# Optimization experiments

Hardware: AMD Instinct MI355X
Metric: run time of the kernel (lower is better)

The kernel has to match this reference:

```python
import jax, jax.numpy as jnp
import numpy as np

HIDDEN = 10
ACTIONS = 6
NUM_LAYERS = 19
IN_CH = 64
LSTM_IN = HIDDEN + 2
EPS = 1e-5
DN = ('NCHW', 'OIHW', 'NCHW')


def _bn(x, g, b):
    # BatchNorm2d in training mode: per-batch stats over (N,H,W), biased variance
    m = x.mean((0, 2, 3), keepdims=True)
    v = x.var((0, 2, 3), keepdims=True)
    return (x - m) * jax.lax.rsqrt(v + EPS) * g[None, :, None, None] + b[None, :, None, None]


def _conv_dw(x, dw_w, ga, ba, pw_w, gb, bb):
    c = x.shape[1]
    x = jax.lax.conv_general_dilated(x, dw_w, (2, 2), [(1, 1), (1, 1)],
                                     feature_group_count=c, dimension_numbers=DN)
    x = jax.nn.relu(_bn(x, ga, ba))
    x = jax.lax.conv_general_dilated(x, pw_w, (1, 1), 'VALID', dimension_numbers=DN)
    return jax.nn.relu(_bn(x, gb, bb))


def _lstm_cell(xt, h, c, wih, whh, bih, bhh):
    # torch gate order: i, f, g, o
    gates = xt @ wih.T + bih + h @ whh.T + bhh
    i, f, g, o = jnp.split(gates, 4, axis=1)
    c = jax.nn.sigmoid(f) * c + jax.nn.sigmoid(i) * jnp.tanh(g)
    h = jax.nn.sigmoid(o) * jnp.tanh(c)
    return h, c


def setup_inputs() -> dict:
    key = jax.random.key(0)
    ks = iter(jax.random.split(key, 32))
    n = lambda shape, s=0.1: jax.random.normal(next(ks), shape, dtype=jnp.float32) * s
    d = {
        'x': jax.random.normal(next(ks), (256, IN_CH, 56, 56), dtype=jnp.float32),
        # block 0: 64 -> 10
        'dw0_w': n((IN_CH, 1, 3, 3)), 'bn0a_g': jnp.ones((IN_CH,)), 'bn0a_b': jnp.zeros((IN_CH,)),
        'pw0_w': n((HIDDEN, IN_CH, 1, 1)), 'bn0b_g': jnp.ones((HIDDEN,)), 'bn0b_b': jnp.zeros((HIDDEN,)),
        # blocks 1..3: 10 -> 10 (stacked)
        'dwr_w': n((3, HIDDEN, 1, 3, 3)), 'bnra_g': jnp.ones((3, HIDDEN)), 'bnra_b': jnp.zeros((3, HIDDEN)),
        'pwr_w': n((3, HIDDEN, HIDDEN, 1, 1)), 'bnrb_g': jnp.ones((3, HIDDEN)), 'bnrb_b': jnp.zeros((3, HIDDEN)),
        # 2-layer LSTM
        'wih0': n((4 * HIDDEN, LSTM_IN)), 'whh0': n((4 * HIDDEN, HIDDEN)),
        'bih0': n((4 * HIDDEN,)), 'bhh0': n((4 * HIDDEN,)),
        'wih1': n((4 * HIDDEN, HIDDEN)), 'whh1': n((4 * HIDDEN, HIDDEN)),
        'bih1': n((4 * HIDDEN,)), 'bhh1': n((4 * HIDDEN,)),
        # hidden2logits
        'head_w': n((2 * ACTIONS, HIDDEN)), 'head_b': n((2 * ACTIONS,)),
    }
    return d


def reference(x, dw0_w, bn0a_g, bn0a_b, pw0_w, bn0b_g, bn0b_b,
              dwr_w, bnra_g, bnra_b, pwr_w, bnrb_g, bnrb_b,
              wih0, whh0, bih0, bhh0, wih1, whh1, bih1, bhh1,
              head_w, head_b):
    # reduce: 4 conv_dw blocks + global avg pool -> [B, HIDDEN]
    f = _conv_dw(x, dw0_w, bn0a_g, bn0a_b, pw0_w, bn0b_g, bn0b_b)
    for i in range(3):
        f = _conv_dw(f, dwr_w[i], bnra_g[i], bnra_b[i], pwr_w[i], bnrb_g[i], bnrb_b[i])
    feat = f.mean((2, 3))  # [B, HIDDEN]
    B = feat.shape[0]
    z = jnp.zeros((B, HIDDEN), feat.dtype)
    key0 = jax.random.key(1)

    def step(carry, _):
        h0, c0, h1, c1, subseq, key = carry
        inp = jnp.concatenate([feat, subseq], axis=1)  # [B, 12]
        h0, c0 = _lstm_cell(inp, h0, c0, wih0, whh0, bih0, bhh0)
        h1, c1 = _lstm_cell(h0, h1, c1, wih1, whh1, bih1, bhh1)
        logits = h1 @ head_w.T + head_b  # [B, 2*ACTIONS]
        logits_a, logits_w = logits[:, :ACTIONS], logits[:, ACTIONS:]
        key, ka, kw = jax.random.split(key, 3)
        bit_a = jax.random.categorical(ka, logits_a, axis=1)
        bit_w = jax.random.categorical(kw, logits_w, axis=1)
        lpa = jnp.take_along_axis(jax.nn.log_softmax(logits_a, axis=1), bit_a[:, None], axis=1)[:, 0]
        lpw = jnp.take_along_axis(jax.nn.log_softmax(logits_w, axis=1), bit_w[:, None], axis=1)[:, 0]
        subseq = jnp.stack([bit_a, bit_w], axis=1).astype(feat.dtype)  # [B, 2]
        return (h0, c0, h1, c1, subseq, key), (bit_a, bit_w, lpa, lpw)

    carry0 = (z, z, z, z, jnp.zeros((B, 2), feat.dtype), key0)
    _, (bit_a, bit_w, lpa, lpw) = jax.lax.scan(step, carry0, None, length=NUM_LAYERS)
    # [T, B] -> [B, T]
    return ((bit_a.T + 2, bit_w.T + 2), (lpa.T, lpw.T))
```

## Files before the change

### kernel.cpp

```cpp
#include <hip/hip_runtime.h>
#include <stdint.h>
#include <math.h>

#define TF_ROUND(r) do { x0 += x1; x1 = (x1 << (r)) | (x1 >> (32 - (r))); x1 ^= x0; } while (0)

__device__ __forceinline__ void threefry2x32(uint32_t k0, uint32_t k1,
                                             uint32_t x0, uint32_t x1,
                                             uint32_t& y0, uint32_t& y1)
{
    uint32_t k2 = k0 ^ k1 ^ 0x1BD11BDAu;
    x0 += k0; x1 += k1;
    TF_ROUND(13); TF_ROUND(15); TF_ROUND(26); TF_ROUND(6);
    x0 += k1; x1 += k2 + 1u;
    TF_ROUND(17); TF_ROUND(29); TF_ROUND(16); TF_ROUND(24);
    x0 += k2; x1 += k0 + 2u;
    TF_ROUND(13); TF_ROUND(15); TF_ROUND(26); TF_ROUND(6);
    x0 += k0; x1 += k1 + 3u;
    TF_ROUND(17); TF_ROUND(29); TF_ROUND(16); TF_ROUND(24);
    x0 += k1; x1 += k2 + 4u;
    TF_ROUND(13); TF_ROUND(15); TF_ROUND(26); TF_ROUND(6);
    y0 = x0 + k2; y1 = x1 + k0 + 5u;
}

__device__ __forceinline__ void wave_red2(double& s, double& q) {
    for (int off = 32; off > 0; off >>= 1) {
        s += __shfl_down(s, off);
        q += __shfl_down(q, off);
    }
}

__device__ __forceinline__ float sigf(float x) { return 0.5f + 0.5f * tanhf(0.5f * x); }

__global__ __launch_bounds__(256) void dw0_kernel(
    const float* __restrict__ in, const float* __restrict__ wts,
    float* __restrict__ out, double* __restrict__ psum)
{
    __shared__ float tile[3136];
    __shared__ double sred[8];
    const int tid = threadIdx.x, lane = tid & 63, wid = tid >> 6;
    const int blk = blockIdx.x;
    const int n = blk >> 6, c = blk & 63;

    const float4* ip4 = (const float4*)(in + (size_t)blk * 3136);
    float4* tp4 = (float4*)tile;
#pragma unroll
    for (int r = 0; r < 3; ++r) tp4[tid + r * 256] = ip4[tid + r * 256];
    if (tid < 16) tp4[768 + tid] = ip4[768 + tid];
    float w9[9];
#pragma unroll
    for (int k = 0; k < 9; ++k) w9[k] = wts[c * 9 + k];
    __syncthreads();

    double ls = 0.0, lq = 0.0;
    if (tid < 196) {
        const int oh = tid / 7, ow0 = (tid - oh * 7) * 4;
        const int col0 = 2 * ow0 - 1;
        float rv[3][9];
#pragma unroll
        for (int kh = 0; kh < 3; ++kh) {
            const int ih = 2 * oh - 1 + kh;
            if (ih >= 0) {
                const float* rp = tile + ih * 56 + col0;
                rv[kh][0] = (col0 >= 0) ? rp[0] : 0.f;
#pragma unroll
                for (int j = 1; j < 9; ++j) rv[kh][j] = rp[j];
            } else {
#pragma unroll
                for (int j = 0; j < 9; ++j) rv[kh][j] = 0.f;
            }
        }
        float a0 = 0.f, a1 = 0.f, a2 = 0.f, a3 = 0.f;
#pragma unroll
        for (int kh = 0; kh < 3; ++kh)
#pragma unroll
            for (int kw = 0; kw < 3; ++kw) {
                const float w = w9[kh * 3 + kw];
                a0 = fmaf(rv[kh][0 + kw], w, a0);
                a1 = fmaf(rv[kh][2 + kw], w, a1);
                a2 = fmaf(rv[kh][4 + kw], w, a2);
                a3 = fmaf(rv[kh][6 + kw], w, a3);
            }
        *(float4*)(out + (size_t)blk * 784 + oh * 28 + ow0) = make_float4(a0, a1, a2, a3);
        ls = (double)a0 + (double)a1 + (double)a2 + (double)a3;
        lq = (double)a0 * a0 + (double)a1 * a1 + (double)a2 * a2 + (double)a3 * a3;
    }
    wave_red2(ls, lq);
    if (lane == 0) { sred[wid] = ls; sred[4 + wid] = lq; }
    __syncthreads();
    if (tid == 0) {
        psum[c * 256 + n] = sred[0] + sred[1] + sred[2] + sred[3];
        psum[16384 + c * 256 + n] = sred[4] + sred[5] + sred[6] + sred[7];
    }
}

__global__ __launch_bounds__(256) void red_chan(
    const double* __restrict__ psum, int NB, double count,
    const float* __restrict__ g, const float* __restrict__ b,
    float2* __restrict__ stats, int C)
{
    __shared__ double sred[8];
    const int c = blockIdx.x, tid = threadIdx.x, lane = tid & 63, wid = tid >> 6;
    double s = 0.0, q = 0.0;
    for (int i = tid; i < NB; i += 256) {
        s += psum[(size_t)c * NB + i];
        q += psum[(size_t)C * NB + (size_t)c * NB + i];
    }
    wave_red2(s, q);
    if (lane == 0) { sred[wid] = s; sred[4 + wid] = q; }
    __syncthreads();
    if (tid == 0) {
        double ss = sred[0] + sred[1] + sred[2] + sred[3];
        double qq = sred[4] + sred[5] + sred[6] + sred[7];
        double mean = ss / count;
        double var = qq / count - mean * mean;
        double A = (1.0 / sqrt(var + 1e-5)) * (double)g[c];
        stats[c] = make_float2((float)A, (float)((double)b[c] - mean * A));
    }
}

__global__ __launch_bounds__(256) void pw0_kernel(
    const float* __restrict__ in, const float* __restrict__ wts,
    const float2* __restrict__ st0, float* __restrict__ out,
    double* __restrict__ psum)
{
    __shared__ float sw[640];
    __shared__ float2 sst[64];
    __shared__ double srs[10][4], srq[10][4];
    const int tid = threadIdx.x, lane = tid & 63, wid = tid >> 6;
    for (int i = tid; i < 640; i += 256) sw[i] = wts[i];
    if (tid < 64) sst[tid] = st0[tid];
    __syncthreads();

    const int p = blockIdx.x * 256 + tid;
    const int n = p / 196, sp4 = p - n * 196;
    const float4* ip4 = (const float4*)in + (size_t)n * 12544 + sp4;
    float4 acc[10];
#pragma unroll
    for (int oc = 0; oc < 10; ++oc) acc[oc] = make_float4(0.f, 0.f, 0.f, 0.f);
#pragma unroll 8
    for (int c = 0; c < 64; ++c) {
        float4 v = ip4[c * 196];
        const float2 stc = sst[c];
        v.x = fmaxf(fmaf(v.x, stc.x, stc.y), 0.f);
        v.y = fmaxf(fmaf(v.y, stc.x, stc.y), 0.f);
        v.z = fmaxf(fmaf(v.z, stc.x, stc.y), 0.f);
        v.w = fmaxf(fmaf(v.w, stc.x, stc.y), 0.f);
#pragma unroll
        for (int oc = 0; oc < 10; ++oc) {
            const float wv = sw[oc * 64 + c];
            acc[oc].x = fmaf(v.x, wv, acc[oc].x);
            acc[oc].y = fmaf(v.y, wv, acc[oc].y);
            acc[oc].z = fmaf(v.z, wv, acc[oc].z);
            acc[oc].w = fmaf(v.w, wv, acc[oc].w);
        }
    }
#pragma unroll
    for (int oc = 0; oc < 10; ++oc)
        ((float4*)out)[(size_t)(n * 10 + oc) * 196 + sp4] = acc[oc];

#pragma unroll
    for (int oc = 0; oc < 10; ++oc) {
        double s = (double)acc[oc].x + (double)acc[oc].y + (double)acc[oc].z + (double)acc[oc].w;
        double q = (double)acc[oc].x * acc[oc].x + (double)acc[oc].y * acc[oc].y
                 + (double)acc[oc].z * acc[oc].z + (double)acc[oc].w * acc[oc].w;
        wave_red2(s, q);
        if (lane == 0) { srs[oc][wid] = s; srq[oc][wid] = q; }
    }
    __syncthreads();
    if (tid < 10) {
        psum[tid * 196 + blockIdx.x] = srs[tid][0] + srs[tid][1] + srs[tid][2] + srs[tid][3];
        psum[1960 + tid * 196 + blockIdx.x] = srq[tid][0] + srq[tid][1] + srq[tid][2] + srq[tid][3];
    }
}

__global__ __launch_bounds__(256) void dw_mid(
    const float* __restrict__ in, const float* __restrict__ wts,
    const float2* __restrict__ stIn, float* __restrict__ out,
    double* __restrict__ psum)
{
    __shared__ float tile[784];
    __shared__ double sred[8];
    const int tid = threadIdx.x, lane = tid & 63, wid = tid >> 6;
    const int blk = blockIdx.x;
    const int n = blk / 10, c = blk - n * 10;
    const float2 stc = stIn[c];
    float w9[9];
#pragma unroll
    for (int k = 0; k < 9; ++k) w9[k] = wts[c * 9 + k];

    const float4* ip4 = (const float4*)(in + (size_t)blk * 784);
    if (tid < 196) {
        float4 v = ip4[tid];
        v.x = fmaxf(fmaf(v.x, stc.x, stc.y), 0.f);
        v.y = fmaxf(fmaf(v.y, stc.x, stc.y), 0.f);
        v.z = fmaxf(fmaf(v.z, stc.x, stc.y), 0.f);
        v.w = fmaxf(fmaf(v.w, stc.x, stc.y), 0.f);
        ((float4*)tile)[tid] = v;
    }
    __syncthreads();

    double ls = 0.0, lq = 0.0;
    if (tid < 196) {
        const int oh = tid / 14, ow = tid - oh * 14;
        float acc = 0.f;
#pragma unroll
        for (int kh = 0; kh < 3; ++kh) {
            const int ih = 2 * oh - 1 + kh;
            if (ih < 0) continue;
#pragma unroll
            for (int kw = 0; kw < 3; ++kw) {
                const int iw = 2 * ow - 1 + kw;
                if (iw < 0) continue;
                acc = fmaf(tile[ih * 28 + iw], w9[kh * 3 + kw], acc);
            }
        }
        out[(size_t)blk * 196 + tid] = acc;
        ls = (double)acc; lq = (double)acc * (double)acc;
    }
    wave_red2(ls, lq);
    if (lane == 0) { sred[wid] = ls; sred[4 + wid] = lq; }
    __syncthreads();
    if (tid == 0) {
        psum[c * 256 + n] = sred[0] + sred[1] + sred[2] + sred[3];
        psum[2560 + c * 256 + n] = sred[4] + sred[5] + sred[6] + sred[7];
    }
}

__global__ __launch_bounds__(256) void pw_mid4(
    const float* __restrict__ in, const float* __restrict__ wts,
    const float2* __restrict__ stIn, float* __restrict__ out,
    double* __restrict__ psum)
{
    __shared__ float sw[100];
    __shared__ float2 sst[10];
    __shared__ double srs[10][4], srq[10][4];
    const int tid = threadIdx.x, lane = tid & 63, wid = tid >> 6;
    if (tid < 100) sw[tid] = wts[tid];
    if (tid < 10) sst[tid] = stIn[tid];
    __syncthreads();

    const int p = blockIdx.x * 256 + tid;
    const int n = p / 49, q = p - n * 49;
    const float4* ip4 = (const float4*)in + (size_t)n * 490 + q;
    float4 acc[10];
#pragma unroll
    for (int oc = 0; oc < 10; ++oc) acc[oc] = make_float4(0.f, 0.f, 0.f, 0.f);
#pragma unroll
    for (int c = 0; c < 10; ++c) {
        float4 v = ip4[c * 49];
        const float2 stc = sst[c];
        v.x = fmaxf(fmaf(v.x, stc.x, stc.y), 0.f);
        v.y = fmaxf(fmaf(v.y, stc.x, stc.y), 0.f);
        v.z = fmaxf(fmaf(v.z, stc.x, stc.y), 0.f);
        v.w = fmaxf(fmaf(v.w, stc.x, stc.y), 0.f);
#pragma unroll
        for (int oc = 0; oc < 10; ++oc) {
            const float wv = sw[oc * 10 + c];
            acc[oc].x = fmaf(v.x, wv, acc[oc].x);
            acc[oc].y = fmaf(v.y, wv, acc[oc].y);
            acc[oc].z = fmaf(v.z, wv, acc[oc].z);
            acc[oc].w = fmaf(v.w, wv, acc[oc].w);
        }
    }
#pragma unroll
    for (int oc = 0; oc < 10; ++oc)
        ((float4*)out)[(size_t)n * 490 + oc * 49 + q] = acc[oc];

#pragma unroll
    for (int oc = 0; oc < 10; ++oc) {
        double s = (double)acc[oc].x + (double)acc[oc].y + (double)acc[oc].z + (double)acc[oc].w;
        double qq = (double)acc[oc].x * acc[oc].x + (double)acc[oc].y * acc[oc].y
                  + (double)acc[oc].z * acc[oc].z + (double)acc[oc].w * acc[oc].w;
        wave_red2(s, qq);
        if (lane == 0) { srs[oc][wid] = s; srq[oc][wid] = qq; }
    }
    __syncthreads();
    if (tid < 10) {
        psum[tid * 49 + blockIdx.x] = srs[tid][0] + srs[tid][1] + srs[tid][2] + srs[tid][3];
        psum[490 + tid * 49 + blockIdx.x] = srq[tid][0] + srq[tid][1] + srq[tid][2] + srq[tid][3];
    }
}

template<int HIN, int HOUT>
__global__ __launch_bounds__(64) void dw_small(
    const float* __restrict__ in, const float* __restrict__ wts,
    const float2* __restrict__ stIn, float* __restrict__ out,
    double* __restrict__ psum)
{
    constexpr int ISZ = HIN * HIN, OSZ = HOUT * HOUT;
    constexpr bool UP = (2 * (HOUT - 1) + 1) >= HIN;
    const int lane = threadIdx.x;
    const int blk = blockIdx.x;
    const int n = blk / 10, c = blk - n * 10;
    const float2 stc = stIn[c];
    float w9[9];
#pragma unroll
    for (int k = 0; k < 9; ++k) w9[k] = wts[c * 9 + k];
    const float* ip = in + (size_t)blk * ISZ;

    double s = 0.0, q = 0.0;
    if (lane < OSZ) {
        const int oh = lane / HOUT, ow = lane - oh * HOUT;
        float acc = 0.f;
#pragma unroll
        for (int kh = 0; kh < 3; ++kh) {
            const int ih = 2 * oh - 1 + kh;
            if (ih < 0) continue;
            if (UP && ih >= HIN) continue;
#pragma unroll
            for (int kw = 0; kw < 3; ++kw) {
                const int iw = 2 * ow - 1 + kw;
                if (iw < 0) continue;
                if (UP && iw >= HIN) continue;
                const float v = fmaxf(fmaf(ip[ih * HIN + iw], stc.x, stc.y), 0.f);
                acc = fmaf(v, w9[kh * 3 + kw], acc);
            }
        }
        out[(size_t)blk * OSZ + lane] = acc;
        s = (double)acc; q = (double)acc * (double)acc;
    }
    wave_red2(s, q);
    if (lane == 0) { psum[c * 256 + n] = s; psum[2560 + c * 256 + n] = q; }
}

template<int S>
__global__ __launch_bounds__(256) void pw_sc(
    const float* __restrict__ in, const float* __restrict__ wts,
    const float2* __restrict__ stIn, float* __restrict__ out,
    double* __restrict__ psum)
{
    __shared__ float sw[100];
    __shared__ float2 sst[10];
    __shared__ double srs[10][4], srq[10][4];
    const int tid = threadIdx.x, lane = tid & 63, wid = tid >> 6;
    if (tid < 100) sw[tid] = wts[tid];
    if (tid < 10) sst[tid] = stIn[tid];
    __syncthreads();

    const int p = blockIdx.x * 256 + tid;
    const int n = p / S, px = p - n * S;
    const float* ip = in + (size_t)n * 10 * S + px;
    float v[10];
#pragma unroll
    for (int c = 0; c < 10; ++c)
        v[c] = fmaxf(fmaf(ip[c * S], sst[c].x, sst[c].y), 0.f);
    float* op = out + (size_t)n * 10 * S + px;
    double ds[10], dq[10];
#pragma unroll
    for (int oc = 0; oc < 10; ++oc) {
        float a = 0.f;
#pragma unroll
        for (int c = 0; c < 10; ++c) a = fmaf(v[c], sw[oc * 10 + c], a);
        op[oc * S] = a;
        ds[oc] = (double)a; dq[oc] = (double)a * (double)a;
    }
#pragma unroll
    for (int oc = 0; oc < 10; ++oc) {
        double s = ds[oc], q = dq[oc];
        wave_red2(s, q);
        if (lane == 0) { srs[oc][wid] = s; srq[oc][wid] = q; }
    }
    __syncthreads();
    if (tid < 10) {
        const int G = gridDim.x;
        psum[tid * G + blockIdx.x] = srs[tid][0] + srs[tid][1] + srs[tid][2] + srs[tid][3];
        psum[10 * G + tid * G + blockIdx.x] = srq[tid][0] + srq[tid][1] + srq[tid][2] + srq[tid][3];
    }
}

__global__ __launch_bounds__(64) void rollout_kernel(
    const float* __restrict__ t7, const float2* __restrict__ st7,
    const float* __restrict__ wih0, const float* __restrict__ whh0,
    const float* __restrict__ bih0, const float* __restrict__ bhh0,
    const float* __restrict__ wih1, const float* __restrict__ whh1,
    const float* __restrict__ bih1, const float* __restrict__ bhh1,
    const float* __restrict__ head_w, const float* __restrict__ head_b,
    float* __restrict__ out)
{
    const int bb = blockIdx.x;
    const int l = threadIdx.x;
    __shared__ float gum[2][19][6];
    __shared__ float s_inp[12], s_h0[10], s_h1[10], s_gates[40], s_logits[12];

    {
        uint32_t k0 = 0u, k1 = 1u;
        const uint32_t m = (uint32_t)(l < 3 ? l : 0);
        for (int t = 0; t < 19; ++t) {
            uint32_t y0, y1;
            threefry2x32(k0, k1, 0u, m, y0, y1);
            const uint32_t nk0 = (uint32_t)__shfl((int)y0, 0);
            const uint32_t nk1 = (uint32_t)__shfl((int)y1, 0);
            const uint32_t ka0 = (uint32_t)__shfl((int)y0, 1);
            const uint32_t ka1 = (uint32_t)__shfl((int)y1, 1);
            const uint32_t kw0 = (uint32_t)__shfl((int)y0, 2);
            const uint32_t kw1 = (uint32_t)__shfl((int)y1, 2);
            if (l < 12) {
                const int path = l / 6;
                const int j = l - path * 6;
                const uint32_t kk0 = path ? kw0 : ka0;
                const uint32_t kk1 = path ? kw1 : ka1;
                const uint32_t flat = (uint32_t)(bb * 6 + j);
                uint32_t z0, z1;
                threefry2x32(kk0, kk1, 0u, flat, z0, z1);
                const uint32_t bits = z0 ^ z1;
                float u = __uint_as_float((bits >> 9) | 0x3f800000u) - 1.0f;
                if (u == 0.0f) u = 1.17549435e-38f;
                const double l1 = log((double)u);
                gum[path][t][j] = (float)(-log(-l1));
            }
            k0 = nk0; k1 = nk1;
        }
    }

    if (l < 10) {
        const float2 stc = st7[l];
        const float* tp = t7 + (size_t)(bb * 10 + l) * 16;
        float f = 0.f;
#pragma unroll
        for (int i = 0; i < 16; ++i) f += fmaxf(fmaf(tp[i], stc.x, stc.y), 0.f);
        s_inp[l] = f * 0.0625f;
        s_h0[l] = 0.f; s_h1[l] = 0.f;
    }
    if (l >= 10 && l < 12) s_inp[l] = 0.f;

    float wi0[12], wh0[10], bs0 = 0.f;
    float wi1[10], wh1[10], bs1 = 0.f;
    float hwr[10], hbr = 0.f;
    if (l < 40) {
#pragma unroll
        for (int k = 0; k < 12; ++k) wi0[k] = wih0[l * 12 + k];
#pragma unroll
        for (int k = 0; k < 10; ++k) wh0[k] = whh0[l * 10 + k];
        bs0 = bih0[l] + bhh0[l];
#pragma unroll
        for (int k = 0; k < 10; ++k) wi1[k] = wih1[l * 10 + k];
#pragma unroll
        for (int k = 0; k < 10; ++k) wh1[k] = whh1[l * 10 + k];
        bs1 = bih1[l] + bhh1[l];
    }
    if (l < 12) {
#pragma unroll
        for (int k = 0; k < 10; ++k) hwr[k] = head_w[l * 10 + k];
        hbr = head_b[l];
    }

    float c0 = 0.f, c1v = 0.f;
    __syncthreads();

    for (int t = 0; t < 19; ++t) {
        if (l < 40) {
            float gacc = bs0;
#pragma unroll
            for (int k = 0; k < 12; ++k) gacc = fmaf(s_inp[k], wi0[k], gacc);
#pragma unroll
            for (int k = 0; k < 10; ++k) gacc = fmaf(s_h0[k], wh0[k], gacc);
            s_gates[l] = gacc;
        }
        __syncthreads();
        if (l < 10) {
            const float gi = s_gates[l], gf = s_gates[10 + l], gg = s_gates[20 + l], go = s_gates[30 + l];
            c0 = sigf(gf) * c0 + sigf(gi) * tanhf(gg);
            s_h0[l] = sigf(go) * tanhf(c0);
        }
        __syncthreads();
        if (l < 40) {
            float gacc = bs1;
#pragma unroll
            for (int k = 0; k < 10; ++k) gacc = fmaf(s_h0[k], wi1[k], gacc);
#pragma unroll
            for (int k = 0; k < 10; ++k) gacc = fmaf(s_h1[k], wh1[k], gacc);
            s_gates[l] = gacc;
        }
        __syncthreads();
        if (l < 10) {
            const float gi = s_gates[l], gf = s_gates[10 + l], gg = s_gates[20 + l], go = s_gates[30 + l];
            c1v = sigf(gf) * c1v + sigf(gi) * tanhf(gg);
            s_h1[l] = sigf(go) * tanhf(c1v);
        }
        __syncthreads();
        if (l < 12) {
            float v = hbr;
#pragma unroll
            for (int k = 0; k < 10; ++k) v = fmaf(s_h1[k], hwr[k], v);
            s_logits[l] = v;
        }
        __syncthreads();
        if (l < 2) {
            const float* lg = &s_logits[l * 6];
            const float* gm = &gum[l][t][0];
            int best = 0; float bv = lg[0] + gm[0];
#pragma unroll
            for (int j = 1; j < 6; ++j) { const float v = lg[j] + gm[j]; if (v > bv) { bv = v; best = j; } }
            float mx = lg[0];
#pragma unroll
            for (int j = 1; j < 6; ++j) mx = fmaxf(mx, lg[j]);
            float se = 0.f;
#pragma unroll
            for (int j = 0; j < 6; ++j) se += expf(lg[j] - mx);
            const float lp = (lg[best] - mx) - logf(se);
            out[l * 4864 + bb * 19 + t] = (float)(best + 2);
            out[9728 + l * 4864 + bb * 19 + t] = lp;
            s_inp[10 + l] = (float)best;
        }
        __syncthreads();
    }
}

extern "C" void kernel_launch(void* const* d_in, const int* in_sizes, int n_in,
                              void* d_out, int out_size, void* d_ws, size_t ws_size,
                              hipStream_t stream)
{
    const float* x      = (const float*)d_in[0];
    const float* dw0_w  = (const float*)d_in[1];
    const float* bn0a_g = (const float*)d_in[2];
    const float* bn0a_b = (const float*)d_in[3];
    const float* pw0_w  = (const float*)d_in[4];
    const float* bn0b_g = (const float*)d_in[5];
    const float* bn0b_b = (const float*)d_in[6];
    const float* dwr_w  = (const float*)d_in[7];
    const float* bnra_g = (const float*)d_in[8];
    const float* bnra_b = (const float*)d_in[9];
    const float* pwr_w  = (const float*)d_in[10];
    const float* bnrb_g = (const float*)d_in[11];
    const float* bnrb_b = (const float*)d_in[12];
    const float* wih0   = (const float*)d_in[13];
    const float* whh0   = (const float*)d_in[14];
    const float* bih0   = (const float*)d_in[15];
    const float* bhh0   = (const float*)d_in[16];
    const float* wih1   = (const float*)d_in[17];
    const float* whh1   = (const float*)d_in[18];
    const float* bih1   = (const float*)d_in[19];
    const float* bhh1   = (const float*)d_in[20];
    const float* head_w = (const float*)d_in[21];
    const float* head_b = (const float*)d_in[22];
    float* out = (float*)d_out;

    char* ws = (char*)d_ws;
    size_t off = 0;
    auto take = [&](size_t bytes) -> char* {
        char* p = ws + off;
        off += (bytes + 255) & ~(size_t)255;
        return p;
    };
    float* y0     = (float*)take(12845056ull * 4);
    float* t1     = (float*)take(2007040ull * 4);
    float* t2     = (float*)take(501760ull * 4);
    float* t3     = (float*)take(501760ull * 4);
    float* t4     = (float*)take(125440ull * 4);
    float* t5     = (float*)take(125440ull * 4);
    float* t6     = (float*)take(40960ull * 4);
    float* t7     = (float*)take(40960ull * 4);
    double* psumA = (double*)take(32768ull * 8);
    double* psumB = (double*)take(3920ull * 8);
    double* psumC = (double*)take(5120ull * 8);
    double* psumD = (double*)take(980ull * 8);
    double* psumE = (double*)take(5120ull * 8);
    double* psumF = (double*)take(980ull * 8);
    double* psumG = (double*)take(5120ull * 8);
    double* psumH = (double*)take(320ull * 8);
    float2* st0   = (float2*)take(64 * sizeof(float2));
    float2* st1   = (float2*)take(16 * sizeof(float2));
    float2* st2   = (float2*)take(16 * sizeof(float2));
    float2* st3   = (float2*)take(16 * sizeof(float2));
    float2* st4   = (float2*)take(16 * sizeof(float2));
    float2* st5   = (float2*)take(16 * sizeof(float2));
    float2* st6   = (float2*)take(16 * sizeof(float2));
    float2* st7   = (float2*)take(16 * sizeof(float2));

    dw0_kernel<<<16384, 256, 0, stream>>>(x, dw0_w, y0, psumA);
    red_chan<<<64, 256, 0, stream>>>(psumA, 256, 200704.0, bn0a_g, bn0a_b, st0, 64);
    pw0_kernel<<<196, 256, 0, stream>>>(y0, pw0_w, st0, t1, psumB);
    red_chan<<<10, 256, 0, stream>>>(psumB, 196, 200704.0, bn0b_g, bn0b_b, st1, 10);
    dw_mid<<<2560, 256, 0, stream>>>(t1, dwr_w, st1, t2, psumC);
    red_chan<<<10, 256, 0, stream>>>(psumC, 256, 50176.0, bnra_g, bnra_b, st2, 10);
    pw_mid4<<<49, 256, 0, stream>>>(t2, pwr_w, st2, t3, psumD);
    red_chan<<<10, 256, 0, stream>>>(psumD, 49, 50176.0, bnrb_g, bnrb_b, st3, 10);
    dw_small<14, 7><<<2560, 64, 0, stream>>>(t3, dwr_w + 90, st3, t4, psumE);
    red_chan<<<10, 256, 0, stream>>>(psumE, 256, 12544.0, bnra_g + 10, bnra_b + 10, st4, 10);
    pw_sc<49><<<49, 256, 0, stream>>>(t4, pwr_w + 100, st4, t5, psumF);
    red_chan<<<10, 256, 0, stream>>>(psumF, 49, 12544.0, bnrb_g + 10, bnrb_b + 10, st5, 10);
    dw_small<7, 4><<<2560, 64, 0, stream>>>(t5, dwr_w + 180, st5, t6, psumG);
    red_chan<<<10, 256, 0, stream>>>(psumG, 256, 4096.0, bnra_g + 20, bnra_b + 20, st6, 10);
    pw_sc<16><<<16, 256, 0, stream>>>(t6, pwr_w + 200, st6, t7, psumH);
    red_chan<<<10, 256, 0, stream>>>(psumH, 16, 4096.0, bnrb_g + 20, bnrb_b + 20, st7, 10);
    rollout_kernel<<<256, 64, 0, stream>>>(t7, st7, wih0, whh0, bih0, bhh0,
                                           wih1, whh1, bih1, bhh1, head_w, head_b, out);
}
```

Baseline: 161.4 us.

## Fold BN statistic reductions into consumer kernels, dropping seven red_chan launches

Each downstream kernel now reduces the producer's per-block partial sums itself and computes the BN scale and shift locally, so the separate red_chan launches between stages go away. This removes seven small kernel launches and their serialization gaps on the stream. In exchange, every block (up to 2560 per stage) redundantly re-reads and reduces up to a few hundred doubles of partial sums, which adds latency at the start of each block.

Measured after the change: 164.6 us. No clear change (+2.0%).

```diff
diff --git a/kernel.cpp b/kernel.cpp
--- a/kernel.cpp
+++ b/kernel.cpp
@@ -173,28 +173,47 @@
     }
 }
 
-__global__ __launch_bounds__(256) void dw_mid(
+__global__ __launch_bounds__(256) void dw_mid_f(
     const float* __restrict__ in, const float* __restrict__ wts,
-    const float2* __restrict__ stIn, float* __restrict__ out,
-    double* __restrict__ psum)
+    const double* __restrict__ psumIn,
+    const float* __restrict__ g, const float* __restrict__ b,
+    float* __restrict__ out, double* __restrict__ psum)
 {
     __shared__ float tile[784];
     __shared__ double sred[8];
+    __shared__ float sAB[2];
     const int tid = threadIdx.x, lane = tid & 63, wid = tid >> 6;
     const int blk = blockIdx.x;
     const int n = blk / 10, c = blk - n * 10;
-    const float2 stc = stIn[c];
+
+    if (wid == 0) {
+        double s = 0.0, q = 0.0;
+        for (int i = lane; i < 196; i += 64) {
+            s += psumIn[c * 196 + i];
+            q += psumIn[1960 + c * 196 + i];
+        }
+        wave_red2(s, q);
+        if (lane == 0) {
+            double mean = s / 200704.0;
+            double var = q / 200704.0 - mean * mean;
+            double A = (1.0 / sqrt(var + 1e-5)) * (double)g[c];
+            sAB[0] = (float)A;
+            sAB[1] = (float)((double)b[c] - mean * A);
+        }
+    }
     float w9[9];
 #pragma unroll
     for (int k = 0; k < 9; ++k) w9[k] = wts[c * 9 + k];
-
+    __syncthreads();
+
+    const float A = sAB[0], B = sAB[1];
     const float4* ip4 = (const float4*)(in + (size_t)blk * 784);
     if (tid < 196) {
         float4 v = ip4[tid];
-        v.x = fmaxf(fmaf(v.x, stc.x, stc.y), 0.f);
-        v.y = fmaxf(fmaf(v.y, stc.x, stc.y), 0.f);
-        v.z = fmaxf(fmaf(v.z, stc.x, stc.y), 0.f);
-        v.w = fmaxf(fmaf(v.w, stc.x, stc.y), 0.f);
+        v.x = fmaxf(fmaf(v.x, A, B), 0.f);
+        v.y = fmaxf(fmaf(v.y, A, B), 0.f);
+        v.z = fmaxf(fmaf(v.z, A, B), 0.f);
+        v.w = fmaxf(fmaf(v.w, A, B), 0.f);
         ((float4*)tile)[tid] = v;
     }
     __syncthreads();
@@ -226,33 +245,47 @@
     }
 }
 
-__global__ __launch_bounds__(256) void pw_mid4(
+__global__ __launch_bounds__(256) void pw_mid4_f(
     const float* __restrict__ in, const float* __restrict__ wts,
-    const float2* __restrict__ stIn, float* __restrict__ out,
-    double* __restrict__ psum)
-{
-    __shared__ float sw[100];
-    __shared__ float2 sst[10];
+    const double* __restrict__ psumIn, double cnt,
+    const float* __restrict__ g, const float* __restrict__ b,
+    float* __restrict__ out, double* __restrict__ psum)
+{
+    __shared__ float sw[100], sA[10], sB[10];
     __shared__ double srs[10][4], srq[10][4];
     const int tid = threadIdx.x, lane = tid & 63, wid = tid >> 6;
     if (tid < 100) sw[tid] = wts[tid];
-    if (tid < 10) sst[tid] = stIn[tid];
+    for (int c = wid; c < 10; c += 4) {
+        double s = 0.0, q = 0.0;
+        for (int i = lane; i < 256; i += 64) {
+            s += psumIn[c * 256 + i];
+            q += psumIn[2560 + c * 256 + i];
+        }
+        wave_red2(s, q);
+        if (lane == 0) {
+            double mean = s / cnt;
+            double var = q / cnt - mean * mean;
+            double A = (1.0 / sqrt(var + 1e-5)) * (double)g[c];
+            sA[c] = (float)A;
+            sB[c] = (float)((double)b[c] - mean * A);
+        }
+    }
     __syncthreads();
 
     const int p = blockIdx.x * 256 + tid;
-    const int n = p / 49, q = p - n * 49;
-    const float4* ip4 = (const float4*)in + (size_t)n * 490 + q;
+    const int n = p / 49, q4 = p - n * 49;
+    const float4* ip4 = (const float4*)in + (size_t)n * 490 + q4;
     float4 acc[10];
 #pragma unroll
     for (int oc = 0; oc < 10; ++oc) acc[oc] = make_float4(0.f, 0.f, 0.f, 0.f);
 #pragma unroll
     for (int c = 0; c < 10; ++c) {
         float4 v = ip4[c * 49];
-        const float2 stc = sst[c];
-        v.x = fmaxf(fmaf(v.x, stc.x, stc.y), 0.f);
-        v.y = fmaxf(fmaf(v.y, stc.x, stc.y), 0.f);
-        v.z = fmaxf(fmaf(v.z, stc.x, stc.y), 0.f);
-        v.w = fmaxf(fmaf(v.w, stc.x, stc.y), 0.f);
+        const float A = sA[c], B = sB[c];
+        v.x = fmaxf(fmaf(v.x, A, B), 0.f);
+        v.y = fmaxf(fmaf(v.y, A, B), 0.f);
+        v.z = fmaxf(fmaf(v.z, A, B), 0.f);
+        v.w = fmaxf(fmaf(v.w, A, B), 0.f);
 #pragma unroll
         for (int oc = 0; oc < 10; ++oc) {
             const float wv = sw[oc * 10 + c];
@@ -264,7 +297,7 @@
     }
 #pragma unroll
     for (int oc = 0; oc < 10; ++oc)
-        ((float4*)out)[(size_t)n * 490 + oc * 49 + q] = acc[oc];
+        ((float4*)out)[(size_t)n * 490 + oc * 49 + q4] = acc[oc];
 
 #pragma unroll
     for (int oc = 0; oc < 10; ++oc) {
@@ -281,24 +314,37 @@
     }
 }
 
-template<int HIN, int HOUT>
-__global__ __launch_bounds__(64) void dw_small(
+template<int HIN, int HOUT, int NBIN>
+__global__ __launch_bounds__(64) void dw_small_f(
     const float* __restrict__ in, const float* __restrict__ wts,
-    const float2* __restrict__ stIn, float* __restrict__ out,
-    double* __restrict__ psum)
+    const double* __restrict__ psumIn, double cnt,
+    const float* __restrict__ g, const float* __restrict__ b,
+    float* __restrict__ out, double* __restrict__ psum)
 {
     constexpr int ISZ = HIN * HIN, OSZ = HOUT * HOUT;
     constexpr bool UP = (2 * (HOUT - 1) + 1) >= HIN;
     const int lane = threadIdx.x;
     const int blk = blockIdx.x;
     const int n = blk / 10, c = blk - n * 10;
-    const float2 stc = stIn[c];
+
+    double s = 0.0, q = 0.0;
+    for (int i = lane; i < NBIN; i += 64) {
+        s += psumIn[c * NBIN + i];
+        q += psumIn[10 * NBIN + c * NBIN + i];
+    }
+    wave_red2(s, q);
+    s = __shfl(s, 0); q = __shfl(q, 0);
+    const double mean = s / cnt;
+    const double var = q / cnt - mean * mean;
+    const double Ad = (1.0 / sqrt(var + 1e-5)) * (double)g[c];
+    const float A = (float)Ad, B = (float)((double)b[c] - mean * Ad);
+
     float w9[9];
 #pragma unroll
     for (int k = 0; k < 9; ++k) w9[k] = wts[c * 9 + k];
     const float* ip = in + (size_t)blk * ISZ;
 
-    double s = 0.0, q = 0.0;
+    double ls = 0.0, lq = 0.0;
     if (lane < OSZ) {
         const int oh = lane / HOUT, ow = lane - oh * HOUT;
         float acc = 0.f;
@@ -312,29 +358,43 @@
                 const int iw = 2 * ow - 1 + kw;
                 if (iw < 0) continue;
                 if (UP && iw >= HIN) continue;
-                const float v = fmaxf(fmaf(ip[ih * HIN + iw], stc.x, stc.y), 0.f);
+                const float v = fmaxf(fmaf(ip[ih * HIN + iw], A, B), 0.f);
                 acc = fmaf(v, w9[kh * 3 + kw], acc);
             }
         }
         out[(size_t)blk * OSZ + lane] = acc;
-        s = (double)acc; q = (double)acc * (double)acc;
-    }
-    wave_red2(s, q);
-    if (lane == 0) { psum[c * 256 + n] = s; psum[2560 + c * 256 + n] = q; }
+        ls = (double)acc; lq = (double)acc * (double)acc;
+    }
+    wave_red2(ls, lq);
+    if (lane == 0) { psum[c * 256 + n] = ls; psum[2560 + c * 256 + n] = lq; }
 }
 
 template<int S>
-__global__ __launch_bounds__(256) void pw_sc(
+__global__ __launch_bounds__(256) void pw_sc_f(
     const float* __restrict__ in, const float* __restrict__ wts,
-    const float2* __restrict__ stIn, float* __restrict__ out,
-    double* __restrict__ psum)
-{
-    __shared__ float sw[100];
-    __shared__ float2 sst[10];
+    const double* __restrict__ psumIn, double cnt,
+    const float* __restrict__ g, const float* __restrict__ b,
+    float* __restrict__ out, double* __restrict__ psum)
+{
+    __shared__ float sw[100], sA[10], sB[10];
     __shared__ double srs[10][4], srq[10][4];
     const int tid = threadIdx.x, lane = tid & 63, wid = tid >> 6;
     if (tid < 100) sw[tid] = wts[tid];
-    if (tid < 10) sst[tid] = stIn[tid];
+    for (int c = wid; c < 10; c += 4) {
+        double s = 0.0, q = 0.0;
+        for (int i = lane; i < 256; i += 64) {
+            s += psumIn[c * 256 + i];
+            q += psumIn[2560 + c * 256 + i];
+        }
+        wave_red2(s, q);
+        if (lane == 0) {
+            double mean = s / cnt;
+            double var = q / cnt - mean * mean;
+            double A = (1.0 / sqrt(var + 1e-5)) * (double)g[c];
+            sA[c] = (float)A;
+            sB[c] = (float)((double)b[c] - mean * A);
+        }
+    }
     __syncthreads();
 
     const int p = blockIdx.x * 256 + tid;
@@ -343,7 +403,7 @@
     float v[10];
 #pragma unroll
     for (int c = 0; c < 10; ++c)
-        v[c] = fmaxf(fmaf(ip[c * S], sst[c].x, sst[c].y), 0.f);
+        v[c] = fmaxf(fmaf(ip[c * S], sA[c], sB[c]), 0.f);
     float* op = out + (size_t)n * 10 * S + px;
     double ds[10], dq[10];
 #pragma unroll
@@ -368,8 +428,9 @@
     }
 }
 
-__global__ __launch_bounds__(64) void rollout_kernel(
-    const float* __restrict__ t7, const float2* __restrict__ st7,
+__global__ __launch_bounds__(64) void rollout_f(
+    const float* __restrict__ t7, const double* __restrict__ psumIn,
+    const float* __restrict__ g, const float* __restrict__ b,
     const float* __restrict__ wih0, const float* __restrict__ whh0,
     const float* __restrict__ bih0, const float* __restrict__ bhh0,
     const float* __restrict__ wih1, const float* __restrict__ whh1,
@@ -413,11 +474,20 @@
     }
 
     if (l < 10) {
-        const float2 stc = st7[l];
+        double s = 0.0, q = 0.0;
+#pragma unroll
+        for (int i = 0; i < 16; ++i) {
+            s += psumIn[l * 16 + i];
+            q += psumIn[160 + l * 16 + i];
+        }
+        const double mean = s / 4096.0;
+        const double var = q / 4096.0 - mean * mean;
+        const double Ad = (1.0 / sqrt(var + 1e-5)) * (double)g[l];
+        const float A = (float)Ad, B = (float)((double)b[l] - mean * Ad);
         const float* tp = t7 + (size_t)(bb * 10 + l) * 16;
         float f = 0.f;
 #pragma unroll
-        for (int i = 0; i < 16; ++i) f += fmaxf(fmaf(tp[i], stc.x, stc.y), 0.f);
+        for (int i = 0; i < 16; ++i) f += fmaxf(fmaf(tp[i], A, B), 0.f);
         s_inp[l] = f * 0.0625f;
         s_h0[l] = 0.f; s_h1[l] = 0.f;
     }
@@ -559,30 +629,21 @@
     double* psumG = (double*)take(5120ull * 8);
     double* psumH = (double*)take(320ull * 8);
     float2* st0   = (float2*)take(64 * sizeof(float2));
-    float2* st1   = (float2*)take(16 * sizeof(float2));
-    float2* st2   = (float2*)take(16 * sizeof(float2));
-    float2* st3   = (float2*)take(16 * sizeof(float2));
-    float2* st4   = (float2*)take(16 * sizeof(float2));
-    float2* st5   = (float2*)take(16 * sizeof(float2));
-    float2* st6   = (float2*)take(16 * sizeof(float2));
-    float2* st7   = (float2*)take(16 * sizeof(float2));
 
     dw0_kernel<<<16384, 256, 0, stream>>>(x, dw0_w, y0, psumA);
     red_chan<<<64, 256, 0, stream>>>(psumA, 256, 200704.0, bn0a_g, bn0a_b, st0, 64);
     pw0_kernel<<<196, 256, 0, stream>>>(y0, pw0_w, st0, t1, psumB);
-    red_chan<<<10, 256, 0, stream>>>(psumB, 196, 200704.0, bn0b_g, bn0b_b, st1, 10);
-    dw_mid<<<2560, 256, 0, stream>>>(t1, dwr_w, st1, t2, psumC);
-    red_chan<<<10, 256, 0, stream>>>(psumC, 256, 50176.0, bnra_g, bnra_b, st2, 10);
-    pw_mid4<<<49, 256, 0, stream>>>(t2, pwr_w, st2, t3, psumD);
-    red_chan<<<10, 256, 0, stream>>>(psumD, 49, 50176.0, bnrb_g, bnrb_b, st3, 10);
-    dw_small<14, 7><<<2560, 64, 0, stream>>>(t3, dwr_w + 90, st3, t4, psumE);
-    red_chan<<<10, 256, 0, stream>>>(psumE, 256, 12544.0, bnra_g + 10, bnra_b + 10, st4, 10);
-    pw_sc<49><<<49, 256, 0, stream>>>(t4, pwr_w + 100, st4, t5, psumF);
-    red_chan<<<10, 256, 0, stream>>>(psumF, 49, 12544.0, bnrb_g + 10, bnrb_b + 10, st5, 10);
-    dw_small<7, 4><<<2560, 64, 0, stream>>>(t5, dwr_w + 180, st5, t6, psumG);
-    red_chan<<<10, 256, 0, stream>>>(psumG, 256, 4096.0, bnra_g + 20, bnra_b + 20, st6, 10);
-    pw_sc<16><<<16, 256, 0, stream>>>(t6, pwr_w + 200, st6, t7, psumH);
-    red_chan<<<10, 256, 0, stream>>>(psumH, 16, 4096.0, bnrb_g + 20, bnrb_b + 20, st7, 10);
-    rollout_kernel<<<256, 64, 0, stream>>>(t7, st7, wih0, whh0, bih0, bhh0,
-                                           wih1, whh1, bih1, bhh1, head_w, head_b, out);
-}
+    dw_mid_f<<<2560, 256, 0, stream>>>(t1, dwr_w, psumB, bn0b_g, bn0b_b, t2, psumC);
+    pw_mid4_f<<<49, 256, 0, stream>>>(t2, pwr_w, psumC, 50176.0, bnra_g, bnra_b, t3, psumD);
+    dw_small_f<14, 7, 49><<<2560, 64, 0, stream>>>(t3, dwr_w + 90, psumD, 50176.0,
+                                                   bnrb_g, bnrb_b, t4, psumE);
+    pw_sc_f<49><<<49, 256, 0, stream>>>(t4, pwr_w + 100, psumE, 12544.0,
+                                        bnra_g + 10, bnra_b + 10, t5, psumF);
+    dw_small_f<7, 4, 49><<<2560, 64, 0, stream>>>(t5, dwr_w + 180, psumF, 12544.0,
+                                                  bnrb_g + 10, bnrb_b + 10, t6, psumG);
+    pw_sc_f<16><<<16, 256, 0, stream>>>(t6, pwr_w + 200, psumG, 4096.0,
+                                        bnra_g + 20, bnra_b + 20, t7, psumH);
+    rollout_f<<<256, 64, 0, stream>>>(t7, psumH, bnrb_g + 20, bnrb_b + 20,
+                                      wih0, whh0, bih0, bhh0, wih1, whh1, bih1, bhh1,
+                                      head_w, head_b, out);
+}
```
